# Performance work log

Hardware: AMD Instinct MI355X
Metric: run time of the kernel (lower is better)

The kernel has to match this reference:

```python
import jax, jax.numpy as jnp
import numpy as np

BD = BH = BW = 4  # block sizes
NH = 8            # num heads


def setup_inputs() -> dict:
    key = jax.random.key(0)
    ks = jax.random.split(key, 5)
    C = 128
    return {
        "x": jax.random.normal(ks[0], (1, C, 30, 62, 126), dtype=jnp.float32),
        "qkv_w": jax.random.normal(ks[1], (3 * C, C), dtype=jnp.float32) * 0.02,
        "qkv_b": jax.random.normal(ks[2], (3 * C,), dtype=jnp.float32) * 0.02,
        "conv_w": jax.random.normal(ks[3], (C, C), dtype=jnp.float32) * 0.02,
        "conv_b": jax.random.normal(ks[4], (C,), dtype=jnp.float32) * 0.02,
    }


def reference(x, qkv_w, qkv_b, conv_w, conv_b):
    B, C, D0, H0, W0 = x.shape
    pad_d = (-D0) % BD
    pad_b = (-H0) % BH
    pad_r = (-W0) % BW
    x = jnp.pad(x, ((0, 0), (0, 0), (0, pad_d), (0, pad_b), (0, pad_r)))
    _, _, D, H, W = x.shape
    d, h, w = D // BD, H // BH, W // BW
    nW, L, hd = d * h * w, BD * BH * BW, C // NH
    scale = hd ** -0.5

    # window partition: (B,C,D,H,W) -> (B, nW, L, C)
    xb = x.reshape(B, C, d, BD, h, BH, w, BW).transpose(0, 2, 4, 6, 3, 5, 7, 1)
    xw = xb.reshape(B, nW, L, C)

    qkv = xw @ qkv_w.T + qkv_b                         # (B,nW,L,3C)
    qkv = qkv.reshape(B, nW, L, 3, NH, hd).transpose(3, 0, 1, 4, 2, 5)
    q, k, v = qkv[0], qkv[1], qkv[2]                   # (B,nW,NH,L,hd)

    attn = jnp.einsum('bnhld,bnhmd->bnhlm', q, k) * scale

    if pad_d > 0 or pad_r > 0 or pad_b > 0:
        mask = jnp.zeros((D, H, W), dtype=x.dtype)
        mask = mask.at[-pad_d:, :, :].set(1.0)
        mask = mask.at[:, -pad_b:, :].set(1.0)
        mask = mask.at[:, :, -pad_r:].set(1.0)
        mask = mask.reshape(d, BD, h, BH, w, BW).transpose(0, 2, 4, 1, 3, 5).reshape(nW, L)
        am = mask[:, None, :] - mask[:, :, None]       # (nW,L,L): mask[j]-mask[i]
        am = jnp.where(am != 0, jnp.asarray(-1000.0, x.dtype), jnp.asarray(0.0, x.dtype))
        attn = attn + am[None, :, None, :, :]

    attn = jax.nn.softmax(attn, axis=-1)
    out = jnp.einsum('bnhlm,bnhmd->bnhld', attn, v)    # (B,nW,NH,L,hd)

    # window merge: -> (B,C,D,H,W)
    out = out.reshape(B, d, h, w, NH, BD, BH, BW, hd)
    out = out.transpose(0, 4, 8, 1, 5, 2, 6, 3, 7).reshape(B, C, D, H, W)
    out = out[:, :, :D0, :H0, :W0]

    # final 1x1x1 conv
    out = jnp.einsum('bcdhw,oc->bodhw', out, conv_w) + conv_b[None, :, None, None, None]
    return out
```

## Files before the change

kernel.cpp:

```cpp
#include <hip/hip_runtime.h>


#define NHEAD 8
#define HDIM 16
#define CCH 128
#define DD0 30
#define HH0 62
#define WW0 126
#define SD 7812
#define SC 234360

typedef __bf16 bfx8 __attribute__((ext_vector_type(8)));
typedef float  fx4  __attribute__((ext_vector_type(4)));
typedef float  fx2  __attribute__((ext_vector_type(2)));

__device__ __forceinline__ fx4 MFMA(bfx8 a, bfx8 b, fx4 c) {
    return __builtin_amdgcn_mfma_f32_16x16x32_bf16(a, b, c, 0, 0, 0);
}
__device__ __forceinline__ fx4 fzero4() { fx4 v = {0.f, 0.f, 0.f, 0.f}; return v; }
__device__ __forceinline__ bfx8 bzero8() {
    bfx8 v;
    #pragma unroll
    for (int j = 0; j < 8; j++) v[j] = (__bf16)0.f;
    return v;
}
__device__ __forceinline__ unsigned pk2(float a, float b) {
    __bf16 ax = (__bf16)a, by = (__bf16)b;
    unsigned short ua = __builtin_bit_cast(unsigned short, ax);
    unsigned short ub = __builtin_bit_cast(unsigned short, by);
    return (unsigned)ua | ((unsigned)ub << 16);
}

__global__ void prep_kernel(const float* __restrict__ qkv_w,
                            const float* __restrict__ conv_w,
                            __bf16* __restrict__ Bq, __bf16* __restrict__ Bc) {
    const int i = blockIdx.x * 256 + threadIdx.x;
    if (i < 49152) Bq[i] = (__bf16)qkv_w[i];
    else            Bc[i - 49152] = (__bf16)conv_w[i - 49152];
}

__global__ __launch_bounds__(256, 4) void winattn_kernel(
    const float* __restrict__ x,
    const float* __restrict__ qkv_b,
    const float* __restrict__ conv_b,
    const __bf16* __restrict__ Bq,
    const __bf16* __restrict__ Bc,
    float* __restrict__ out)
{
    __shared__ __align__(16) unsigned char lds_raw[32768];
    __bf16* ldsQ = (__bf16*)lds_raw;
    __bf16* ldsK = (__bf16*)(lds_raw + 16384);

    const int tid  = threadIdx.x;
    const int wave = tid >> 6;
    const int lane = tid & 63;
    const int quad = lane >> 4;
    const int l15  = lane & 15;

    const int blk = blockIdx.x;
    const int wid = ((blk & 7) << 9) | (blk >> 3);
    const int Db = (wid >> 9) << 2;
    const int Hb = ((wid >> 5) & 15) << 2;
    const int Wb = (wid & 31) << 2;

    unsigned long long pmask;
    {
        const bool p = (Db + (lane >> 4) >= DD0) || (Hb + ((lane >> 2) & 3) >= HH0) ||
                       (Wb + (lane & 3) >= WW0);
        pmask = __ballot(p);
    }

    {
        #pragma unroll
        for (int it = 0; it < 16; it++) {
            const int u = it * 256 + tid;
            const int wp = u & 1;
            const int dh = (u >> 1) & 15;
            const int c  = u >> 5;
            const int Dg = Db + (dh >> 2), Hg = Hb + (dh & 3);
            const bool valid = (Dg < DD0) && (Hg < HH0) && (wp == 0 || Wb < 124);
            fx2 v = {0.f, 0.f};
            if (valid) v = *(const fx2*)(x + c * SC + Dg * SD + Hg * WW0 + Wb + wp * 2);
            const int tok0 = dh * 4 + wp * 2;
            ldsQ[tok0 * 128 + (((c >> 3) ^ (tok0 & 15)) << 3) + (c & 7)] = (__bf16)v[0];
            const int tok1 = tok0 + 1;
            ldsQ[tok1 * 128 + (((c >> 3) ^ (tok1 & 15)) << 3) + (c & 7)] = (__bf16)v[1];
        }
    }
    __syncthreads();

    unsigned vpk[2][4][2];

    {
        fx4 acc[4][4];
        #pragma unroll
        for (int mt = 0; mt < 4; mt++)
            #pragma unroll
            for (int j = 0; j < 4; j++) acc[mt][j] = fzero4();
        #pragma unroll
        for (int ks = 0; ks < 4; ks++) {
            bfx8 a[4];
            #pragma unroll
            for (int mt = 0; mt < 4; mt++) {
                const int m = mt * 16 + l15;
                const int phys = (ks * 4 + quad) ^ (m & 15);
                a[mt] = *(const bfx8*)(ldsQ + m * 128 + phys * 8);
            }
            #pragma unroll
            for (int j = 0; j < 4; j++) {
                const int col = (1 + (j >> 1)) * 128 + (wave + (j & 1) * 4) * 16 + l15;
                const bfx8 bb = *(const bfx8*)(Bq + (col * 16 + ks * 4 + quad) * 8);
                #pragma unroll
                for (int mt = 0; mt < 4; mt++) acc[mt][j] = MFMA(a[mt], bb, acc[mt][j]);
            }
        }
        #pragma unroll
        for (int j = 0; j < 2; j++) {
            const int hh = wave + j * 4;
            const float bias = qkv_b[128 + hh * 16 + l15];
            #pragma unroll
            for (int mt = 0; mt < 4; mt++)
                #pragma unroll
                for (int r = 0; r < 4; r++) {
                    const int tok = mt * 16 + quad * 4 + r;
                    const int phys = (l15 >> 3) ^ ((tok >> 2) & 1);
                    ldsK[hh * 1024 + tok * 16 + phys * 8 + (l15 & 7)] =
                        (__bf16)(acc[mt][j][r] + bias);
                }
        }
        #pragma unroll
        for (int hi = 0; hi < 2; hi++) {
            const float bias = qkv_b[256 + (wave + hi * 4) * 16 + l15];
            #pragma unroll
            for (int mt = 0; mt < 4; mt++) {
                vpk[hi][mt][0] = pk2(acc[mt][2 + hi][0] + bias, acc[mt][2 + hi][1] + bias);
                vpk[hi][mt][1] = pk2(acc[mt][2 + hi][2] + bias, acc[mt][2 + hi][3] + bias);
            }
        }
    }

    {
        fx4 acc[4][2];
        #pragma unroll
        for (int mt = 0; mt < 4; mt++)
            #pragma unroll
            for (int hi = 0; hi < 2; hi++) acc[mt][hi] = fzero4();
        #pragma unroll
        for (int ks = 0; ks < 4; ks++) {
            bfx8 a[4];
            #pragma unroll
            for (int mt = 0; mt < 4; mt++) {
                const int m = mt * 16 + l15;
                const int phys = (ks * 4 + quad) ^ (m & 15);
                a[mt] = *(const bfx8*)(ldsQ + m * 128 + phys * 8);
            }
            #pragma unroll
            for (int hi = 0; hi < 2; hi++) {
                const int col = (wave + hi * 4) * 16 + l15;
                const bfx8 bb = *(const bfx8*)(Bq + (col * 16 + ks * 4 + quad) * 8);
                #pragma unroll
                for (int mt = 0; mt < 4; mt++) acc[mt][hi] = MFMA(a[mt], bb, acc[mt][hi]);
            }
        }
        __syncthreads();
        #pragma unroll
        for (int hi = 0; hi < 2; hi++) {
            const int hh = wave + hi * 4;
            const float bias = qkv_b[hh * 16 + l15];
            #pragma unroll
            for (int mt = 0; mt < 4; mt++)
                #pragma unroll
                for (int r = 0; r < 4; r++) {
                    const int tok = mt * 16 + quad * 4 + r;
                    const int phys = (l15 >> 3) ^ ((tok >> 2) & 1);
                    ldsQ[hh * 1024 + tok * 16 + phys * 8 + (l15 & 7)] =
                        (__bf16)((acc[mt][hi][r] + bias) * 0.25f);
                }
        }
    }
    __syncthreads();

    const int srcA = ((((quad << 1) + 0) & 3) << 4) | l15;
    const int srcB = ((((quad << 1) + 1) & 3) << 4) | l15;
    #pragma unroll
    for (int hi = 0; hi < 2; hi++) {
        const int hh = wave + hi * 4;
        __bf16* qs = ldsQ + hh * 1024;
        __bf16* kk = ldsK + hh * 1024;

        fx4 lg[4][4];
        #pragma unroll
        for (int mt = 0; mt < 4; mt++)
            #pragma unroll
            for (int nt = 0; nt < 4; nt++) lg[mt][nt] = fzero4();

        bfx8 aq[4];
        #pragma unroll
        for (int mt = 0; mt < 4; mt++) {
            aq[mt] = bzero8();
            if (quad < 2) {
                const int m = mt * 16 + l15;
                const int phys = quad ^ ((m >> 2) & 1);
                aq[mt] = *(const bfx8*)(qs + m * 16 + phys * 8);
            }
        }
        #pragma unroll
        for (int nt = 0; nt < 4; nt++) {
            bfx8 bk = bzero8();
            if (quad < 2) {
                const int n = nt * 16 + l15;
                const int phys = quad ^ ((n >> 2) & 1);
                bk = *(const bfx8*)(kk + n * 16 + phys * 8);
            }
            #pragma unroll
            for (int mt = 0; mt < 4; mt++) lg[mt][nt] = MFMA(aq[mt], bk, lg[mt][nt]);
        }

        #pragma unroll
        for (int mt = 0; mt < 4; mt++) {
            float sum[4] = {0.f, 0.f, 0.f, 0.f};
            #pragma unroll
            for (int nt = 0; nt < 4; nt++) {
                const unsigned cb = (unsigned)(pmask >> (nt * 16 + l15)) & 1u;
                #pragma unroll
                for (int r = 0; r < 4; r++) {
                    const unsigned rb = (unsigned)(pmask >> (mt * 16 + quad * 4 + r)) & 1u;
                    const float e = (rb ^ cb) ? 0.f : __expf(lg[mt][nt][r]);
                    lg[mt][nt][r] = e;
                    sum[r] += e;
                }
            }
            #pragma unroll
            for (int r = 0; r < 4; r++) {
                float s = sum[r];
                s += __shfl_xor(s, 1);
                s += __shfl_xor(s, 2);
                s += __shfl_xor(s, 4);
                s += __shfl_xor(s, 8);
                const float rinv = __builtin_amdgcn_rcpf(s);
                #pragma unroll
                for (int nt = 0; nt < 4; nt++) lg[mt][nt][r] *= rinv;
            }
        }

        fx4 ovec[4];
        #pragma unroll
        for (int mt = 0; mt < 4; mt++) ovec[mt] = fzero4();
        #pragma unroll
        for (int half = 0; half < 2; half++) {
            #pragma unroll
            for (int nn = 0; nn < 2; nn++) {
                __bf16* piece = nn ? kk : qs;
                const int nt = half * 2 + nn;
                #pragma unroll
                for (int mt = 0; mt < 4; mt++)
                    #pragma unroll
                    for (int r = 0; r < 4; r++) {
                        const int tok = mt * 16 + quad * 4 + r;
                        const int phys = (l15 >> 3) ^ ((tok >> 2) & 1);
                        piece[tok * 16 + phys * 8 + (l15 & 7)] = (__bf16)lg[mt][nt][r];
                    }
            }
            const unsigned a00 = (unsigned)__shfl((int)vpk[hi][half * 2 + 0][0], srcA);
            const unsigned a01 = (unsigned)__shfl((int)vpk[hi][half * 2 + 0][1], srcA);
            const unsigned a10 = (unsigned)__shfl((int)vpk[hi][half * 2 + 1][0], srcA);
            const unsigned a11 = (unsigned)__shfl((int)vpk[hi][half * 2 + 1][1], srcA);
            const unsigned b00 = (unsigned)__shfl((int)vpk[hi][half * 2 + 0][0], srcB);
            const unsigned b01 = (unsigned)__shfl((int)vpk[hi][half * 2 + 0][1], srcB);
            const unsigned b10 = (unsigned)__shfl((int)vpk[hi][half * 2 + 1][0], srcB);
            const unsigned b11 = (unsigned)__shfl((int)vpk[hi][half * 2 + 1][1], srcB);
            const bool mhi = quad >= 2;
            uint4 uv;
            uv.x = mhi ? a10 : a00;
            uv.y = mhi ? a11 : a01;
            uv.z = mhi ? b10 : b00;
            uv.w = mhi ? b11 : b01;
            const bfx8 bv = __builtin_bit_cast(bfx8, uv);
            #pragma unroll
            for (int mt = 0; mt < 4; mt++) {
                const int m = mt * 16 + l15;
                const int phys = (quad & 1) ^ ((m >> 2) & 1);
                const bfx8 ap = *(const bfx8*)(((quad >> 1) ? kk : qs) + m * 16 + phys * 8);
                ovec[mt] = MFMA(ap, bv, ovec[mt]);
            }
        }
        #pragma unroll
        for (int mt = 0; mt < 4; mt++)
            #pragma unroll
            for (int r = 0; r < 4; r++) {
                const int tok = mt * 16 + quad * 4 + r;
                const int phys = (l15 >> 3) ^ ((tok >> 2) & 1);
                qs[tok * 16 + phys * 8 + (l15 & 7)] = (__bf16)ovec[mt][r];
            }
    }
    __syncthreads();

    {
        fx4 cacc[4][2];
        #pragma unroll
        for (int mt = 0; mt < 4; mt++)
            #pragma unroll
            for (int nt = 0; nt < 2; nt++) cacc[mt][nt] = fzero4();
        #pragma unroll
        for (int ks = 0; ks < 4; ks++) {
            const int kg = ks * 4 + quad;
            bfx8 a[4];
            #pragma unroll
            for (int mt = 0; mt < 4; mt++) {
                const int m = mt * 16 + l15;
                const int phys = (kg & 1) ^ ((m >> 2) & 1);
                a[mt] = *(const bfx8*)(ldsQ + (kg >> 1) * 1024 + m * 16 + phys * 8);
            }
            #pragma unroll
            for (int nt = 0; nt < 2; nt++) {
                const int o = wave * 32 + nt * 16 + l15;
                const bfx8 bb = *(const bfx8*)(Bc + (o * 16 + kg) * 8);
                #pragma unroll
                for (int mt = 0; mt < 4; mt++) cacc[mt][nt] = MFMA(a[mt], bb, cacc[mt][nt]);
            }
        }
        #pragma unroll
        for (int nt = 0; nt < 2; nt++) {
            const int o = wave * 32 + nt * 16 + l15;
            const float cb = conv_b[o];
            #pragma unroll
            for (int mt = 0; mt < 4; mt++) {
                if (Db + mt < DD0) {
                    const int Hg = Hb + quad;
                    if (Hg < HH0) {
                        const int base = o * SC + (Db + mt) * SD + Hg * WW0 + Wb;
                        fx2 w0 = {cacc[mt][nt][0] + cb, cacc[mt][nt][1] + cb};
                        *(fx2*)(out + base) = w0;
                        if (Wb < 124) {
                            fx2 w1 = {cacc[mt][nt][2] + cb, cacc[mt][nt][3] + cb};
                            *(fx2*)(out + base + 2) = w1;
                        }
                    }
                }
            }
        }
    }
}

extern "C" void kernel_launch(void* const* d_in, const int* in_sizes, int n_in,
                              void* d_out, int out_size, void* d_ws, size_t ws_size,
                              hipStream_t stream) {
    const float* x      = (const float*)d_in[0];
    const float* qkv_w  = (const float*)d_in[1];
    const float* qkv_b  = (const float*)d_in[2];
    const float* conv_w = (const float*)d_in[3];
    const float* conv_b = (const float*)d_in[4];
    float* out = (float*)d_out;

    __bf16* Bq = (__bf16*)d_ws;
    __bf16* Bc = (__bf16*)((char*)d_ws + 98304);

    prep_kernel<<<256, 256, 0, stream>>>(qkv_w, conv_w, Bq, Bc);
    winattn_kernel<<<4096, 256, 0, stream>>>(x, qkv_b, conv_b, Bq, Bc, out);
}
```

Measured before the change: 441.3 us.

## Keep Q/K/V in registers with transposed MFMA fragments; shrink LDS

Restructures the fused window-attention kernel so Q, K and V projections land directly in register fragments in transposed (head-dim-as-K) layout. Scores and PV are computed with 16-element-K MFMA calls that zero-pad the upper half, and the softmax row reduction now uses two cross-quad shuffles instead of four. The per-head LDS round-trips and V shuffles are gone, LDS drops to 20 KB, and conv weights are pre-permuted so the output conv reads a register-friendly layout. The catch is that half of each MFMA's K lanes are wasted on zero padding, and the output stores become scalar per-element writes strided by channel instead of fx2 vector stores.

```diff
diff --git a/kernel.cpp b/kernel.cpp
--- a/kernel.cpp
+++ b/kernel.cpp
@@ -1,9 +1,6 @@
 #include <hip/hip_runtime.h>
 
 
-#define NHEAD 8
-#define HDIM 16
-#define CCH 128
 #define DD0 30
 #define HH0 62
 #define WW0 126
@@ -18,11 +15,11 @@
     return __builtin_amdgcn_mfma_f32_16x16x32_bf16(a, b, c, 0, 0, 0);
 }
 __device__ __forceinline__ fx4 fzero4() { fx4 v = {0.f, 0.f, 0.f, 0.f}; return v; }
-__device__ __forceinline__ bfx8 bzero8() {
-    bfx8 v;
-    #pragma unroll
-    for (int j = 0; j < 8; j++) v[j] = (__bf16)0.f;
-    return v;
+
+__device__ __forceinline__ fx4 MFMA16(uint2 a, uint2 b, fx4 c) {
+    uint4 ua; ua.x = a.x; ua.y = a.y; ua.z = 0u; ua.w = 0u;
+    uint4 ub; ub.x = b.x; ub.y = b.y; ub.z = 0u; ub.w = 0u;
+    return MFMA(__builtin_bit_cast(bfx8, ua), __builtin_bit_cast(bfx8, ub), c);
 }
 __device__ __forceinline__ unsigned pk2(float a, float b) {
     __bf16 ax = (__bf16)a, by = (__bf16)b;
@@ -33,10 +30,16 @@
 
 __global__ void prep_kernel(const float* __restrict__ qkv_w,
                             const float* __restrict__ conv_w,
-                            __bf16* __restrict__ Bq, __bf16* __restrict__ Bc) {
+                            __bf16* __restrict__ Bq, __bf16* __restrict__ Bc2) {
     const int i = blockIdx.x * 256 + threadIdx.x;
-    if (i < 49152) Bq[i] = (__bf16)qkv_w[i];
-    else            Bc[i - 49152] = (__bf16)conv_w[i - 49152];
+    if (i < 49152) {
+        Bq[i] = (__bf16)qkv_w[i];
+    } else {
+        const int t = i - 49152;
+        const int o  = (t >> 2) & 127;
+        const int ch = ((t >> 9) << 2) | (t & 3);
+        Bc2[t] = (__bf16)conv_w[o * 128 + ch];
+    }
 }
 
 __global__ __launch_bounds__(256, 4) void winattn_kernel(
@@ -44,12 +47,12 @@
     const float* __restrict__ qkv_b,
     const float* __restrict__ conv_b,
     const __bf16* __restrict__ Bq,
-    const __bf16* __restrict__ Bc,
+    const __bf16* __restrict__ Bc2,
     float* __restrict__ out)
 {
-    __shared__ __align__(16) unsigned char lds_raw[32768];
-    __bf16* ldsQ = (__bf16*)lds_raw;
-    __bf16* ldsK = (__bf16*)(lds_raw + 16384);
+    __shared__ __align__(16) unsigned char lds_raw[20480];
+    __bf16* ldsX = (__bf16*)lds_raw;
+    __bf16* ldsO = (__bf16*)lds_raw;
 
     const int tid  = threadIdx.x;
     const int wave = tid >> 6;
@@ -82,261 +85,158 @@
             fx2 v = {0.f, 0.f};
             if (valid) v = *(const fx2*)(x + c * SC + Dg * SD + Hg * WW0 + Wb + wp * 2);
             const int tok0 = dh * 4 + wp * 2;
-            ldsQ[tok0 * 128 + (((c >> 3) ^ (tok0 & 15)) << 3) + (c & 7)] = (__bf16)v[0];
+            ldsX[tok0 * 128 + (((c >> 3) ^ (tok0 & 15)) << 3) + (c & 7)] = (__bf16)v[0];
             const int tok1 = tok0 + 1;
-            ldsQ[tok1 * 128 + (((c >> 3) ^ (tok1 & 15)) << 3) + (c & 7)] = (__bf16)v[1];
+            ldsX[tok1 * 128 + (((c >> 3) ^ (tok1 & 15)) << 3) + (c & 7)] = (__bf16)v[1];
         }
     }
     __syncthreads();
 
-    unsigned vpk[2][4][2];
-
-    {
-        fx4 acc[4][4];
-        #pragma unroll
-        for (int mt = 0; mt < 4; mt++)
-            #pragma unroll
-            for (int j = 0; j < 4; j++) acc[mt][j] = fzero4();
-        #pragma unroll
-        for (int ks = 0; ks < 4; ks++) {
-            bfx8 a[4];
-            #pragma unroll
-            for (int mt = 0; mt < 4; mt++) {
-                const int m = mt * 16 + l15;
-                const int phys = (ks * 4 + quad) ^ (m & 15);
-                a[mt] = *(const bfx8*)(ldsQ + m * 128 + phys * 8);
-            }
-            #pragma unroll
-            for (int j = 0; j < 4; j++) {
-                const int col = (1 + (j >> 1)) * 128 + (wave + (j & 1) * 4) * 16 + l15;
-                const bfx8 bb = *(const bfx8*)(Bq + (col * 16 + ks * 4 + quad) * 8);
-                #pragma unroll
-                for (int mt = 0; mt < 4; mt++) acc[mt][j] = MFMA(a[mt], bb, acc[mt][j]);
-            }
-        }
-        #pragma unroll
-        for (int j = 0; j < 2; j++) {
-            const int hh = wave + j * 4;
-            const float bias = qkv_b[128 + hh * 16 + l15];
-            #pragma unroll
-            for (int mt = 0; mt < 4; mt++)
-                #pragma unroll
-                for (int r = 0; r < 4; r++) {
-                    const int tok = mt * 16 + quad * 4 + r;
-                    const int phys = (l15 >> 3) ^ ((tok >> 2) & 1);
-                    ldsK[hh * 1024 + tok * 16 + phys * 8 + (l15 & 7)] =
-                        (__bf16)(acc[mt][j][r] + bias);
+    uint2 qf[2][4], kf[2][4], vf[2][4];
+    #pragma unroll
+    for (int pair = 0; pair < 2; pair++) {
+        bfx8 X[2][4];
+        #pragma unroll
+        for (int t = 0; t < 2; t++)
+            #pragma unroll
+            for (int kk = 0; kk < 4; kk++) {
+                const int m = (pair * 2 + t) * 16 + l15;
+                const int phys = (kk * 4 + quad) ^ (m & 15);
+                X[t][kk] = *(const bfx8*)(ldsX + m * 128 + phys * 8);
+            }
+        #pragma unroll
+        for (int s = 0; s < 6; s++) {
+            const int hi = s >> 1 >= 1 ? (s >= 3 ? 1 : 0) : 0;
+            const int kind = s < 3 ? s : s - 3;
+            const int h = wave + ((s < 3) ? 0 : 4);
+            const int colbase = kind * 128 + h * 16;
+            fx4 acc[2];
+            acc[0] = fzero4(); acc[1] = fzero4();
+            #pragma unroll
+            for (int kk = 0; kk < 4; kk++) {
+                const bfx8 Wf = *(const bfx8*)(Bq + ((colbase + l15) * 16 + kk * 4 + quad) * 8);
+                #pragma unroll
+                for (int t = 0; t < 2; t++)
+                    acc[t] = (kind == 2) ? MFMA(X[t][kk], Wf, acc[t])
+                                         : MFMA(Wf, X[t][kk], acc[t]);
+            }
+            const int hidx = (s < 3) ? 0 : 1;
+            #pragma unroll
+            for (int t = 0; t < 2; t++) {
+                const int tile = pair * 2 + t;
+                if (kind == 2) {
+                    const float b = qkv_b[colbase + l15];
+                    uint2 f;
+                    f.x = pk2(acc[t][0] + b, acc[t][1] + b);
+                    f.y = pk2(acc[t][2] + b, acc[t][3] + b);
+                    vf[hidx][tile] = f;
+                } else {
+                    float v0 = acc[t][0] + qkv_b[colbase + 4 * quad + 0];
+                    float v1 = acc[t][1] + qkv_b[colbase + 4 * quad + 1];
+                    float v2 = acc[t][2] + qkv_b[colbase + 4 * quad + 2];
+                    float v3 = acc[t][3] + qkv_b[colbase + 4 * quad + 3];
+                    if (kind == 0) { v0 *= 0.25f; v1 *= 0.25f; v2 *= 0.25f; v3 *= 0.25f; }
+                    uint2 f;
+                    f.x = pk2(v0, v1);
+                    f.y = pk2(v2, v3);
+                    if (kind == 0) qf[hidx][tile] = f; else kf[hidx][tile] = f;
                 }
-        }
-        #pragma unroll
-        for (int hi = 0; hi < 2; hi++) {
-            const float bias = qkv_b[256 + (wave + hi * 4) * 16 + l15];
-            #pragma unroll
-            for (int mt = 0; mt < 4; mt++) {
-                vpk[hi][mt][0] = pk2(acc[mt][2 + hi][0] + bias, acc[mt][2 + hi][1] + bias);
-                vpk[hi][mt][1] = pk2(acc[mt][2 + hi][2] + bias, acc[mt][2 + hi][3] + bias);
-            }
-        }
-    }
-
-    {
-        fx4 acc[4][2];
-        #pragma unroll
-        for (int mt = 0; mt < 4; mt++)
-            #pragma unroll
-            for (int hi = 0; hi < 2; hi++) acc[mt][hi] = fzero4();
-        #pragma unroll
-        for (int ks = 0; ks < 4; ks++) {
-            bfx8 a[4];
-            #pragma unroll
-            for (int mt = 0; mt < 4; mt++) {
-                const int m = mt * 16 + l15;
-                const int phys = (ks * 4 + quad) ^ (m & 15);
-                a[mt] = *(const bfx8*)(ldsQ + m * 128 + phys * 8);
-            }
-            #pragma unroll
-            for (int hi = 0; hi < 2; hi++) {
-                const int col = (wave + hi * 4) * 16 + l15;
-                const bfx8 bb = *(const bfx8*)(Bq + (col * 16 + ks * 4 + quad) * 8);
-                #pragma unroll
-                for (int mt = 0; mt < 4; mt++) acc[mt][hi] = MFMA(a[mt], bb, acc[mt][hi]);
-            }
-        }
-        __syncthreads();
-        #pragma unroll
-        for (int hi = 0; hi < 2; hi++) {
-            const int hh = wave + hi * 4;
-            const float bias = qkv_b[hh * 16 + l15];
-            #pragma unroll
-            for (int mt = 0; mt < 4; mt++)
-                #pragma unroll
-                for (int r = 0; r < 4; r++) {
-                    const int tok = mt * 16 + quad * 4 + r;
-                    const int phys = (l15 >> 3) ^ ((tok >> 2) & 1);
-                    ldsQ[hh * 1024 + tok * 16 + phys * 8 + (l15 & 7)] =
-                        (__bf16)((acc[mt][hi][r] + bias) * 0.25f);
-                }
+            }
         }
     }
     __syncthreads();
 
-    const int srcA = ((((quad << 1) + 0) & 3) << 4) | l15;
-    const int srcB = ((((quad << 1) + 1) & 3) << 4) | l15;
+    unsigned mBv[4], mAv[4];
+    #pragma unroll
+    for (int i = 0; i < 4; i++) {
+        mBv[i] = (unsigned)((pmask >> (16 * i + l15)) & 1ull);
+        mAv[i] = (unsigned)((pmask >> (16 * i + 4 * quad)) & 0xFull);
+    }
+
     #pragma unroll
     for (int hi = 0; hi < 2; hi++) {
-        const int hh = wave + hi * 4;
-        __bf16* qs = ldsQ + hh * 1024;
-        __bf16* kk = ldsK + hh * 1024;
-
-        fx4 lg[4][4];
-        #pragma unroll
-        for (int mt = 0; mt < 4; mt++)
-            #pragma unroll
-            for (int nt = 0; nt < 4; nt++) lg[mt][nt] = fzero4();
-
-        bfx8 aq[4];
-        #pragma unroll
-        for (int mt = 0; mt < 4; mt++) {
-            aq[mt] = bzero8();
-            if (quad < 2) {
-                const int m = mt * 16 + l15;
-                const int phys = quad ^ ((m >> 2) & 1);
-                aq[mt] = *(const bfx8*)(qs + m * 16 + phys * 8);
-            }
-        }
+        const int h = wave + hi * 4;
+        fx4 ot[4];
+        #pragma unroll
+        for (int i = 0; i < 4; i++) ot[i] = fzero4();
+        #pragma unroll
+        for (int tau = 0; tau < 4; tau++) {
+            fx4 stc[4];
+            #pragma unroll
+            for (int nu = 0; nu < 4; nu++)
+                stc[nu] = MFMA16(kf[hi][nu], qf[hi][tau], fzero4());
+            float sum = 0.f;
+            const unsigned bm = mBv[tau];
+            #pragma unroll
+            for (int nu = 0; nu < 4; nu++)
+                #pragma unroll
+                for (int r = 0; r < 4; r++) {
+                    const unsigned am = (mAv[nu] >> r) & 1u;
+                    const float e = (am ^ bm) ? 0.f : __expf(stc[nu][r]);
+                    stc[nu][r] = e;
+                    sum += e;
+                }
+            sum += __shfl_xor(sum, 16);
+            sum += __shfl_xor(sum, 32);
+            const float rinv = __builtin_amdgcn_rcpf(sum);
+            #pragma unroll
+            for (int nu = 0; nu < 4; nu++) {
+                uint2 pf;
+                pf.x = pk2(stc[nu][0] * rinv, stc[nu][1] * rinv);
+                pf.y = pk2(stc[nu][2] * rinv, stc[nu][3] * rinv);
+                ot[tau] = MFMA16(vf[hi][nu], pf, ot[tau]);
+            }
+        }
+        #pragma unroll
+        for (int tau = 0; tau < 4; tau++) {
+            uint2 w;
+            w.x = pk2(ot[tau][0], ot[tau][1]);
+            w.y = pk2(ot[tau][2], ot[tau][3]);
+            *(uint2*)(ldsO + h * 1280 + (16 * tau + l15) * 20 + 4 * quad) = w;
+        }
+    }
+    __syncthreads();
+
+    {
+        fx4 cacc[2][4];
+        #pragma unroll
+        for (int t = 0; t < 2; t++)
+            #pragma unroll
+            for (int nt = 0; nt < 4; nt++) cacc[t][nt] = fzero4();
+        #pragma unroll
+        for (int h = 0; h < 8; h++) {
+            uint2 bfr[4], afr[2];
+            #pragma unroll
+            for (int nt = 0; nt < 4; nt++)
+                bfr[nt] = *(const uint2*)(ldsO + h * 1280 + (16 * nt + l15) * 20 + 4 * quad);
+            #pragma unroll
+            for (int t = 0; t < 2; t++)
+                afr[t] = *(const uint2*)(Bc2 + (((h * 4 + quad) * 128) + (wave * 2 + t) * 16 + l15) * 4);
+            #pragma unroll
+            for (int t = 0; t < 2; t++)
+                #pragma unroll
+                for (int nt = 0; nt < 4; nt++)
+                    cacc[t][nt] = MFMA16(afr[t], bfr[nt], cacc[t][nt]);
+        }
+        const int bh = l15 >> 2, bw = l15 & 3;
+        float cb[2][4];
+        #pragma unroll
+        for (int t = 0; t < 2; t++)
+            #pragma unroll
+            for (int r = 0; r < 4; r++)
+                cb[t][r] = conv_b[(wave * 2 + t) * 16 + 4 * quad + r];
         #pragma unroll
         for (int nt = 0; nt < 4; nt++) {
-            bfx8 bk = bzero8();
-            if (quad < 2) {
-                const int n = nt * 16 + l15;
-                const int phys = quad ^ ((n >> 2) & 1);
-                bk = *(const bfx8*)(kk + n * 16 + phys * 8);
-            }
-            #pragma unroll
-            for (int mt = 0; mt < 4; mt++) lg[mt][nt] = MFMA(aq[mt], bk, lg[mt][nt]);
-        }
-
-        #pragma unroll
-        for (int mt = 0; mt < 4; mt++) {
-            float sum[4] = {0.f, 0.f, 0.f, 0.f};
-            #pragma unroll
-            for (int nt = 0; nt < 4; nt++) {
-                const unsigned cb = (unsigned)(pmask >> (nt * 16 + l15)) & 1u;
-                #pragma unroll
-                for (int r = 0; r < 4; r++) {
-                    const unsigned rb = (unsigned)(pmask >> (mt * 16 + quad * 4 + r)) & 1u;
-                    const float e = (rb ^ cb) ? 0.f : __expf(lg[mt][nt][r]);
-                    lg[mt][nt][r] = e;
-                    sum[r] += e;
-                }
-            }
-            #pragma unroll
-            for (int r = 0; r < 4; r++) {
-                float s = sum[r];
-                s += __shfl_xor(s, 1);
-                s += __shfl_xor(s, 2);
-                s += __shfl_xor(s, 4);
-                s += __shfl_xor(s, 8);
-                const float rinv = __builtin_amdgcn_rcpf(s);
-                #pragma unroll
-                for (int nt = 0; nt < 4; nt++) lg[mt][nt][r] *= rinv;
-            }
-        }
-
-        fx4 ovec[4];
-        #pragma unroll
-        for (int mt = 0; mt < 4; mt++) ovec[mt] = fzero4();
-        #pragma unroll
-        for (int half = 0; half < 2; half++) {
-            #pragma unroll
-            for (int nn = 0; nn < 2; nn++) {
-                __bf16* piece = nn ? kk : qs;
-                const int nt = half * 2 + nn;
-                #pragma unroll
-                for (int mt = 0; mt < 4; mt++)
-                    #pragma unroll
-                    for (int r = 0; r < 4; r++) {
-                        const int tok = mt * 16 + quad * 4 + r;
-                        const int phys = (l15 >> 3) ^ ((tok >> 2) & 1);
-                        piece[tok * 16 + phys * 8 + (l15 & 7)] = (__bf16)lg[mt][nt][r];
-                    }
-            }
-            const unsigned a00 = (unsigned)__shfl((int)vpk[hi][half * 2 + 0][0], srcA);
-            const unsigned a01 = (unsigned)__shfl((int)vpk[hi][half * 2 + 0][1], srcA);
-            const unsigned a10 = (unsigned)__shfl((int)vpk[hi][half * 2 + 1][0], srcA);
-            const unsigned a11 = (unsigned)__shfl((int)vpk[hi][half * 2 + 1][1], srcA);
-            const unsigned b00 = (unsigned)__shfl((int)vpk[hi][half * 2 + 0][0], srcB);
-            const unsigned b01 = (unsigned)__shfl((int)vpk[hi][half * 2 + 0][1], srcB);
-            const unsigned b10 = (unsigned)__shfl((int)vpk[hi][half * 2 + 1][0], srcB);
-            const unsigned b11 = (unsigned)__shfl((int)vpk[hi][half * 2 + 1][1], srcB);
-            const bool mhi = quad >= 2;
-            uint4 uv;
-            uv.x = mhi ? a10 : a00;
-            uv.y = mhi ? a11 : a01;
-            uv.z = mhi ? b10 : b00;
-            uv.w = mhi ? b11 : b01;
-            const bfx8 bv = __builtin_bit_cast(bfx8, uv);
-            #pragma unroll
-            for (int mt = 0; mt < 4; mt++) {
-                const int m = mt * 16 + l15;
-                const int phys = (quad & 1) ^ ((m >> 2) & 1);
-                const bfx8 ap = *(const bfx8*)(((quad >> 1) ? kk : qs) + m * 16 + phys * 8);
-                ovec[mt] = MFMA(ap, bv, ovec[mt]);
-            }
-        }
-        #pragma unroll
-        for (int mt = 0; mt < 4; mt++)
-            #pragma unroll
-            for (int r = 0; r < 4; r++) {
-                const int tok = mt * 16 + quad * 4 + r;
-                const int phys = (l15 >> 3) ^ ((tok >> 2) & 1);
-                qs[tok * 16 + phys * 8 + (l15 & 7)] = (__bf16)ovec[mt][r];
-            }
-    }
-    __syncthreads();
-
-    {
-        fx4 cacc[4][2];
-        #pragma unroll
-        for (int mt = 0; mt < 4; mt++)
-            #pragma unroll
-            for (int nt = 0; nt < 2; nt++) cacc[mt][nt] = fzero4();
-        #pragma unroll
-        for (int ks = 0; ks < 4; ks++) {
-            const int kg = ks * 4 + quad;
-            bfx8 a[4];
-            #pragma unroll
-            for (int mt = 0; mt < 4; mt++) {
-                const int m = mt * 16 + l15;
-                const int phys = (kg & 1) ^ ((m >> 2) & 1);
-                a[mt] = *(const bfx8*)(ldsQ + (kg >> 1) * 1024 + m * 16 + phys * 8);
-            }
-            #pragma unroll
-            for (int nt = 0; nt < 2; nt++) {
-                const int o = wave * 32 + nt * 16 + l15;
-                const bfx8 bb = *(const bfx8*)(Bc + (o * 16 + kg) * 8);
-                #pragma unroll
-                for (int mt = 0; mt < 4; mt++) cacc[mt][nt] = MFMA(a[mt], bb, cacc[mt][nt]);
-            }
-        }
-        #pragma unroll
-        for (int nt = 0; nt < 2; nt++) {
-            const int o = wave * 32 + nt * 16 + l15;
-            const float cb = conv_b[o];
-            #pragma unroll
-            for (int mt = 0; mt < 4; mt++) {
-                if (Db + mt < DD0) {
-                    const int Hg = Hb + quad;
-                    if (Hg < HH0) {
-                        const int base = o * SC + (Db + mt) * SD + Hg * WW0 + Wb;
-                        fx2 w0 = {cacc[mt][nt][0] + cb, cacc[mt][nt][1] + cb};
-                        *(fx2*)(out + base) = w0;
-                        if (Wb < 124) {
-                            fx2 w1 = {cacc[mt][nt][2] + cb, cacc[mt][nt][3] + cb};
-                            *(fx2*)(out + base + 2) = w1;
-                        }
-                    }
-                }
+            const int Dg = Db + nt;
+            const bool ok = (Dg < DD0) && (Hb + bh < HH0) && (Wb + bw < WW0);
+            if (!ok) continue;
+            const int base_sp = Dg * SD + (Hb + bh) * WW0 + (Wb + bw);
+            #pragma unroll
+            for (int t = 0; t < 2; t++) {
+                const int o0 = (wave * 2 + t) * 16 + 4 * quad;
+                #pragma unroll
+                for (int r = 0; r < 4; r++)
+                    out[(o0 + r) * SC + base_sp] = cacc[t][nt][r] + cb[t][r];
             }
         }
     }
@@ -352,9 +252,9 @@
     const float* conv_b = (const float*)d_in[4];
     float* out = (float*)d_out;
 
-    __bf16* Bq = (__bf16*)d_ws;
-    __bf16* Bc = (__bf16*)((char*)d_ws + 98304);
-
-    prep_kernel<<<256, 256, 0, stream>>>(qkv_w, conv_w, Bq, Bc);
-    winattn_kernel<<<4096, 256, 0, stream>>>(x, qkv_b, conv_b, Bq, Bc, out);
-}
+    __bf16* Bq  = (__bf16*)d_ws;
+    __bf16* Bc2 = (__bf16*)((char*)d_ws + 98304);
+
+    prep_kernel<<<256, 256, 0, stream>>>(qkv_w, conv_w, Bq, Bc2);
+    winattn_kernel<<<4096, 256, 0, stream>>>(x, qkv_b, conv_b, Bq, Bc2, out);
+}
```

Result: no change. 449.8 us (+1.9%).
